# Optimization experiments

Measured on AMD Instinct MI355X. Metric: run time of the kernel, lower is better.

The kernel has to match this reference:

```python
import jax, jax.numpy as jnp
import numpy as np
from jax import lax

MARGIN = 0.3
BIGF = 1e9


def _pairwise_dist(x):
    # dist[i,j] = ||x_i - x_j||, clamped at 1e-12 before sqrt (as in torch code)
    sq = jnp.sum(x * x, axis=1)
    d = sq[:, None] + sq[None, :] - 2.0 * (x @ x.T)
    return jnp.sqrt(jnp.clip(d, 1e-12))


def _hard_mining(dist, targets):
    is_pos = targets[:, None] == targets[None, :]
    ap = jnp.where(is_pos, dist, jnp.asarray(-BIGF, dist.dtype))
    an = jnp.where(is_pos, jnp.asarray(BIGF, dist.dtype), dist)
    dist_ap = jnp.max(ap, axis=1)
    p_inds = jnp.argmax(ap, axis=1)
    dist_an = jnp.min(an, axis=1)
    n_inds = jnp.argmin(an, axis=1)
    return dist_ap, dist_an, p_inds, n_inds


def _batch_euclidean(x, y):
    # x: [N,m,d], y: [N,n,d] -> [N,m,n]
    xx = jnp.sum(x * x, axis=-1)[:, :, None]
    yy = jnp.sum(y * y, axis=-1)[:, None, :]
    d = xx + yy - 2.0 * jnp.einsum('nmd,nkd->nmk', x, y)
    return jnp.sqrt(jnp.clip(d, 1e-12))


def _shortest_dist(dmat):
    # DTW-style shortest path over [m,n] grid, batched over N: dp[i,j] = d[i,j] + min(dp[i-1,j], dp[i,j-1])
    N, m, n = dmat.shape
    big = jnp.asarray(BIGF, dmat.dtype)
    init_row = jnp.full((N, n), big, dmat.dtype).at[:, 0].set(0.0)  # virtual row -1: only (0,0) reachable

    def row_step(prev_row, drow):  # prev_row,drow: [N,n]
        def col_step(left, un):  # left: [N]
            up, d = un
            cur = d + jnp.minimum(up, left)
            return cur, cur
        _, cols = lax.scan(col_step, jnp.full((N,), big, dmat.dtype), (prev_row.T, drow.T))
        return cols.T, None

    last_row, _ = lax.scan(row_step, init_row, jnp.moveaxis(dmat, 1, 0))
    return last_row[:, -1]


def _batch_local_dist(x, y):
    d = _batch_euclidean(x, y)
    d = jnp.tanh(d * 0.5)  # == (exp(d)-1)/(exp(d)+1), numerically safe
    return _shortest_dist(d)


def _margin_ranking(dist_an, dist_ap, margin):
    # MarginRankingLoss with y=1: mean(relu(margin - (dist_an - dist_ap)))
    return jnp.mean(jnp.maximum(0.0, margin + dist_ap - dist_an))


def setup_inputs() -> dict:
    key = jax.random.key(0)
    k1, k2 = jax.random.split(key)
    N, D = 512, 2048
    LD, PARTS = 128, 8
    K = 4  # instances per identity (PK sampling)
    inputs = jax.random.normal(k1, (N, D), dtype=jnp.float32)
    local_features = jax.random.normal(k2, (N, LD, PARTS), dtype=jnp.float32)
    targets = jnp.arange(N, dtype=jnp.int64) // K
    return {"inputs": inputs, "targets": targets, "local_features": local_features}


def reference(inputs, targets, local_features):
    dist = _pairwise_dist(inputs)
    dist_ap, dist_an, p_inds, n_inds = _hard_mining(dist, targets)
    global_loss = _margin_ranking(dist_an, dist_ap, MARGIN)
    lf = jnp.transpose(local_features, (0, 2, 1))  # [N, parts, local_dim]
    local_ap = _batch_local_dist(lf, lf[p_inds])
    local_an = _batch_local_dist(lf, lf[n_inds])
    local_loss = _margin_ranking(local_an, local_ap, MARGIN)
    return (global_loss, local_loss)
```

## Files before the change

### kernel.cpp

```cpp
#include <hip/hip_runtime.h>
#include <math.h>

#define MARGIN 0.3f
#define BIGF 1e9f
#define NN 512
#define DD 2048
#define LDIM 128
#define PARTS 8

__global__ __launch_bounds__(256) void k_norms_init(
    const float* __restrict__ X, float* __restrict__ norms,
    float* gsum, float* lsum, unsigned* counter)
{
    int i = blockIdx.x;
    int t = threadIdx.x;
    const float4* xr = (const float4*)(X + (size_t)i * DD);
    float4 v1 = xr[t];
    float4 v2 = xr[t + 256];
    float acc = v1.x * v1.x + v1.y * v1.y + v1.z * v1.z + v1.w * v1.w
              + v2.x * v2.x + v2.y * v2.y + v2.z * v2.z + v2.w * v2.w;
    for (int off = 32; off > 0; off >>= 1)
        acc += __shfl_down(acc, off);
    __shared__ float part[4];
    int lane = t & 63, wid = t >> 6;
    if (lane == 0) part[wid] = acc;
    __syncthreads();
    if (t == 0) {
        norms[i] = part[0] + part[1] + part[2] + part[3];
        if (i == 0) { *gsum = 0.0f; *lsum = 0.0f; *counter = 0u; }
    }
}

__global__ __launch_bounds__(256) void k_gram(
    const float* __restrict__ X, float* __restrict__ Gp)
{
    __shared__ float As[16][64];
    __shared__ float Bs[16][64];
    int bid = blockIdx.x;
    int tj = bid & 7;
    int ti = (bid >> 3) & 7;
    int ks = bid >> 6;
    int tid = threadIdx.x;

    int lr = tid >> 2;
    int lc = (tid & 3) << 2;
    const float* Ap = X + (size_t)(ti * 64 + lr) * DD;
    const float* Bp = X + (size_t)(tj * 64 + lr) * DD;

    int ty = tid >> 4;
    int tx = tid & 15;

    float acc[4][4];
#pragma unroll
    for (int r = 0; r < 4; r++)
#pragma unroll
        for (int c = 0; c < 4; c++) acc[r][c] = 0.0f;

    int k0 = ks * 512;
    for (int kc = 0; kc < 32; kc++) {
        float4 av = *(const float4*)(Ap + k0 + lc);
        float4 bv = *(const float4*)(Bp + k0 + lc);
        __syncthreads();
        As[lc + 0][lr] = av.x; As[lc + 1][lr] = av.y;
        As[lc + 2][lr] = av.z; As[lc + 3][lr] = av.w;
        Bs[lc + 0][lr] = bv.x; Bs[lc + 1][lr] = bv.y;
        Bs[lc + 2][lr] = bv.z; Bs[lc + 3][lr] = bv.w;
        __syncthreads();
#pragma unroll
        for (int kk = 0; kk < 16; kk++) {
            float4 a4 = *(const float4*)&As[kk][ty << 2];
            float4 b4 = *(const float4*)&Bs[kk][tx << 2];
            float ar[4] = {a4.x, a4.y, a4.z, a4.w};
            float br[4] = {b4.x, b4.y, b4.z, b4.w};
#pragma unroll
            for (int r = 0; r < 4; r++)
#pragma unroll
                for (int c = 0; c < 4; c++)
                    acc[r][c] = fmaf(ar[r], br[c], acc[r][c]);
        }
        k0 += 16;
    }

    float* outp = Gp + (size_t)ks * NN * NN
                + (size_t)(ti * 64 + (ty << 2)) * NN + tj * 64 + (tx << 2);
#pragma unroll
    for (int r = 0; r < 4; r++) {
        float4 v = make_float4(acc[r][0], acc[r][1], acc[r][2], acc[r][3]);
        *(float4*)(outp + (size_t)r * NN) = v;
    }
}

__global__ __launch_bounds__(256) void k_mining(
    const float* __restrict__ Gp, const float* __restrict__ norms,
    const int* __restrict__ tg, int* __restrict__ p_inds,
    int* __restrict__ n_inds, float* gsum)
{
    int i = blockIdx.x;
    int t = threadIdx.x;
    float ni = norms[i];
    int tgt_i = tg[i];

    float apv = -BIGF; int api = 0x7fffffff;
    float anv =  BIGF; int ani = 0x7fffffff;

#pragma unroll
    for (int jj = 0; jj < 2; jj++) {
        int j = t + jj * 256;
        size_t base = (size_t)i * NN + j;
        float g = Gp[base] + Gp[base + (size_t)NN * NN]
                + Gp[base + 2ul * NN * NN] + Gp[base + 3ul * NN * NN];
        float dd = ni + norms[j] - 2.0f * g;
        float dist = sqrtf(fmaxf(dd, 1e-12f));
        bool pos = (tg[j] == tgt_i);
        float a = pos ? dist : -BIGF;
        if (a > apv || (a == apv && j < api)) { apv = a; api = j; }
        float b = pos ? BIGF : dist;
        if (b < anv || (b == anv && j < ani)) { anv = b; ani = j; }
    }
    for (int off = 32; off > 0; off >>= 1) {
        float av = __shfl_down(apv, off); int ai = __shfl_down(api, off);
        if (av > apv || (av == apv && ai < api)) { apv = av; api = ai; }
        float nv = __shfl_down(anv, off); int nid = __shfl_down(ani, off);
        if (nv < anv || (nv == anv && nid < ani)) { anv = nv; ani = nid; }
    }
    __shared__ float s_apv[4]; __shared__ int s_api[4];
    __shared__ float s_anv[4]; __shared__ int s_ani[4];
    int lane = t & 63, wid = t >> 6;
    if (lane == 0) { s_apv[wid] = apv; s_api[wid] = api;
                     s_anv[wid] = anv; s_ani[wid] = ani; }
    __syncthreads();
    if (t == 0) {
        apv = s_apv[0]; api = s_api[0]; anv = s_anv[0]; ani = s_ani[0];
        for (int wv = 1; wv < 4; wv++) {
            float av = s_apv[wv]; int ai = s_api[wv];
            if (av > apv || (av == apv && ai < api)) { apv = av; api = ai; }
            float nv = s_anv[wv]; int nid = s_ani[wv];
            if (nv < anv || (nv == anv && nid < ani)) { anv = nv; ani = nid; }
        }
        p_inds[i] = api;
        n_inds[i] = ani;
        atomicAdd(gsum, fmaxf(0.0f, MARGIN + apv - anv));
    }
}

__global__ __launch_bounds__(128) void k_local(
    const float* __restrict__ LF, const int* __restrict__ p_inds,
    const int* __restrict__ n_inds, const float* gsum, float* lsum,
    unsigned* counter, float* __restrict__ out)
{
    int i = blockIdx.x;
    int tid = threadIdx.x;
    int w = tid >> 6;
    int lane = tid & 63;

    __shared__ float A[LDIM * PARTS];
    __shared__ float B[2][LDIM * PARTS];
    __shared__ float dtm[2][64];
    __shared__ float res[2];

    const float4* A4 = (const float4*)(LF + (size_t)i * LDIM * PARTS);
    ((float4*)A)[tid]        = A4[tid];
    ((float4*)A)[tid + 128]  = A4[tid + 128];

    int ind = (w == 0) ? p_inds[i] : n_inds[i];
    const float4* B4 = (const float4*)(LF + (size_t)ind * LDIM * PARTS);
    float4* Bw = (float4*)B[w];
    Bw[lane]        = B4[lane];
    Bw[lane + 64]   = B4[lane + 64];
    Bw[lane + 128]  = B4[lane + 128];
    Bw[lane + 192]  = B4[lane + 192];
    __syncthreads();

    int p = lane >> 3, q = lane & 7;
    float acc = 0.0f;
    const float* Bl = B[w];
    for (int d = 0; d < LDIM; d++) {
        float diff = A[d * PARTS + p] - Bl[d * PARTS + q];
        acc = fmaf(diff, diff, acc);
    }
    float dist = sqrtf(fmaxf(acc, 1e-12f));
    dtm[w][p * 8 + q] = tanhf(0.5f * dist);
    __syncthreads();

    if (lane == 0) {
        const float* dm = dtm[w];
        float dp[8];
        dp[0] = dm[0];
        for (int j = 1; j < 8; j++) dp[j] = dp[j - 1] + dm[j];
        for (int r = 1; r < 8; r++) {
            dp[0] += dm[r * 8];
            for (int j = 1; j < 8; j++)
                dp[j] = dm[r * 8 + j] + fminf(dp[j], dp[j - 1]);
        }
        res[w] = dp[7];
    }
    __syncthreads();

    if (tid == 0) {
        float l = fmaxf(0.0f, MARGIN + res[0] - res[1]);
        atomicAdd(lsum, l);
        __threadfence();
        unsigned old = atomicAdd(counter, 1u);
        if (old == (NN - 1)) {
            float ls = atomicAdd(lsum, 0.0f);
            out[0] = (*(volatile const float*)gsum) * (1.0f / NN);
            out[1] = ls * (1.0f / NN);
        }
    }
}

extern "C" void kernel_launch(void* const* d_in, const int* in_sizes, int n_in,
                              void* d_out, int out_size, void* d_ws, size_t ws_size,
                              hipStream_t stream)
{
    const float* X  = (const float*)d_in[0];
    const int*   tg = (const int*)d_in[1];
    const float* LF = (const float*)d_in[2];
    float* out = (float*)d_out;

    char* ws = (char*)d_ws;
    float*    Gp      = (float*)ws;
    float*    norms   = (float*)(ws + 4194304);
    int*      p_inds  = (int*)  (ws + 4196352);
    int*      n_inds  = (int*)  (ws + 4198400);
    float*    gsum    = (float*)(ws + 4200448);
    float*    lsum    = (float*)(ws + 4200452);
    unsigned* counter = (unsigned*)(ws + 4200456);

    k_norms_init<<<NN, 256, 0, stream>>>(X, norms, gsum, lsum, counter);
    k_gram<<<256, 256, 0, stream>>>(X, Gp);
    k_mining<<<NN, 256, 0, stream>>>(Gp, norms, tg, p_inds, n_inds, gsum);
    k_local<<<NN, 128, 0, stream>>>(LF, p_inds, n_inds, gsum, lsum, counter, out);
}
```

Before: 115.2 us.

## Compute Gram matrix with split-bf16 MFMA and fuse mining with local loss

Input features are split into bf16 hi/lo parts in the prep kernel, and the Gram matrix is computed with 16x16x32 bf16 MFMA instructions using three products (hi*hi, hi*lo, lo*hi) to approximate fp32 accuracy. Tiles are loaded straight into LDS with global_load_lds. The mining and local-distance kernels are merged into one launch, so the p/n indices stay in shared memory and one kernel launch is removed. In exchange the prep kernel writes extra bf16 buffers, and the split-bf16 product is a small precision approximation of the fp32 Gram matrix.

```diff
diff --git a/kernel.cpp b/kernel.cpp
--- a/kernel.cpp
+++ b/kernel.cpp
@@ -8,9 +8,19 @@
 #define LDIM 128
 #define PARTS 8
 
-__global__ __launch_bounds__(256) void k_norms_init(
-    const float* __restrict__ X, float* __restrict__ norms,
-    float* gsum, float* lsum, unsigned* counter)
+typedef __attribute__((ext_vector_type(8))) __bf16 bf16x8;
+typedef __attribute__((ext_vector_type(4))) __bf16 bf16x4;
+typedef __attribute__((ext_vector_type(4))) float f32x4;
+
+__device__ __forceinline__ void load_lds16(const void* g, void* lds) {
+    __builtin_amdgcn_global_load_lds(
+        (const __attribute__((address_space(1))) unsigned int*)g,
+        (__attribute__((address_space(3))) unsigned int*)lds, 16, 0, 0);
+}
+
+__global__ __launch_bounds__(256) void k_prep(
+    const float* __restrict__ X, __bf16* __restrict__ Hhi, __bf16* __restrict__ Hlo,
+    float* __restrict__ norms, float* gsum, float* lsum, unsigned* counter)
 {
     int i = blockIdx.x;
     int t = threadIdx.x;
@@ -19,6 +29,24 @@
     float4 v2 = xr[t + 256];
     float acc = v1.x * v1.x + v1.y * v1.y + v1.z * v1.z + v1.w * v1.w
               + v2.x * v2.x + v2.y * v2.y + v2.z * v2.z + v2.w * v2.w;
+
+    float e1[4] = {v1.x, v1.y, v1.z, v1.w};
+    float e2[4] = {v2.x, v2.y, v2.z, v2.w};
+    bf16x4 h1, h2, l1, l2;
+#pragma unroll
+    for (int j = 0; j < 4; j++) {
+        __bf16 h = (__bf16)e1[j];
+        h1[j] = h;
+        l1[j] = (__bf16)(e1[j] - (float)h);
+        __bf16 g = (__bf16)e2[j];
+        h2[j] = g;
+        l2[j] = (__bf16)(e2[j] - (float)g);
+    }
+    bf16x4* hr = (bf16x4*)(Hhi + (size_t)i * DD);
+    bf16x4* lr = (bf16x4*)(Hlo + (size_t)i * DD);
+    hr[t] = h1; hr[t + 256] = h2;
+    lr[t] = l1; lr[t + 256] = l2;
+
     for (int off = 32; off > 0; off >>= 1)
         acc += __shfl_down(acc, off);
     __shared__ float part[4];
@@ -31,70 +59,98 @@
     }
 }
 
-__global__ __launch_bounds__(256) void k_gram(
-    const float* __restrict__ X, float* __restrict__ Gp)
-{
-    __shared__ float As[16][64];
-    __shared__ float Bs[16][64];
+__global__ __launch_bounds__(256) void k_gram_mfma(
+    const __bf16* __restrict__ Hhi, const __bf16* __restrict__ Hlo,
+    float* __restrict__ Gp)
+{
+    __shared__ __bf16 Ah[2048], Al[2048], Bh[2048], Bl[2048];
+
     int bid = blockIdx.x;
     int tj = bid & 7;
     int ti = (bid >> 3) & 7;
     int ks = bid >> 6;
-    int tid = threadIdx.x;
-
-    int lr = tid >> 2;
-    int lc = (tid & 3) << 2;
-    const float* Ap = X + (size_t)(ti * 64 + lr) * DD;
-    const float* Bp = X + (size_t)(tj * 64 + lr) * DD;
-
-    int ty = tid >> 4;
-    int tx = tid & 15;
-
-    float acc[4][4];
-#pragma unroll
-    for (int r = 0; r < 4; r++)
-#pragma unroll
-        for (int c = 0; c < 4; c++) acc[r][c] = 0.0f;
-
-    int k0 = ks * 512;
-    for (int kc = 0; kc < 32; kc++) {
-        float4 av = *(const float4*)(Ap + k0 + lc);
-        float4 bv = *(const float4*)(Bp + k0 + lc);
+    int t = threadIdx.x;
+    int w = t >> 6, lane = t & 63;
+    int wr = w >> 1, wc = w & 1;
+
+    int row16 = (w << 4) + (lane & 15);
+    int kchunk = (lane >> 4) << 3;
+    size_t kc0 = (size_t)(ks * 512 + kchunk);
+    const __bf16* pAh = Hhi + (size_t)(ti * 64 + row16) * DD + kc0;
+    const __bf16* pAl = Hlo + (size_t)(ti * 64 + row16) * DD + kc0;
+    const __bf16* pBh = Hhi + (size_t)(tj * 64 + row16) * DD + kc0;
+    const __bf16* pBl = Hlo + (size_t)(tj * 64 + row16) * DD + kc0;
+    __bf16* ldsAh = &Ah[w * 512];
+    __bf16* ldsAl = &Al[w * 512];
+    __bf16* ldsBh = &Bh[w * 512];
+    __bf16* ldsBl = &Bl[w * 512];
+
+    f32x4 acc00 = {0.f, 0.f, 0.f, 0.f};
+    f32x4 acc01 = {0.f, 0.f, 0.f, 0.f};
+    f32x4 acc10 = {0.f, 0.f, 0.f, 0.f};
+    f32x4 acc11 = {0.f, 0.f, 0.f, 0.f};
+
+    for (int it = 0; it < 16; ++it) {
+        load_lds16(pAh, ldsAh);
+        load_lds16(pBh, ldsBh);
+        load_lds16(pAl, ldsAl);
+        load_lds16(pBl, ldsBl);
+        pAh += 32; pAl += 32; pBh += 32; pBl += 32;
         __syncthreads();
-        As[lc + 0][lr] = av.x; As[lc + 1][lr] = av.y;
-        As[lc + 2][lr] = av.z; As[lc + 3][lr] = av.w;
-        Bs[lc + 0][lr] = bv.x; Bs[lc + 1][lr] = bv.y;
-        Bs[lc + 2][lr] = bv.z; Bs[lc + 3][lr] = bv.w;
+
+        const bf16x8* fAh = (const bf16x8*)&Ah[wr * 1024];
+        const bf16x8* fAl = (const bf16x8*)&Al[wr * 1024];
+        const bf16x8* fBh = (const bf16x8*)&Bh[wc * 1024];
+        const bf16x8* fBl = (const bf16x8*)&Bl[wc * 1024];
+        bf16x8 ah0 = fAh[lane], ah1 = fAh[lane + 64];
+        bf16x8 al0 = fAl[lane], al1 = fAl[lane + 64];
+        bf16x8 bh0 = fBh[lane], bh1 = fBh[lane + 64];
+        bf16x8 bl0 = fBl[lane], bl1 = fBl[lane + 64];
+
+        acc00 = __builtin_amdgcn_mfma_f32_16x16x32_bf16(ah0, bh0, acc00, 0, 0, 0);
+        acc00 = __builtin_amdgcn_mfma_f32_16x16x32_bf16(ah0, bl0, acc00, 0, 0, 0);
+        acc00 = __builtin_amdgcn_mfma_f32_16x16x32_bf16(al0, bh0, acc00, 0, 0, 0);
+
+        acc01 = __builtin_amdgcn_mfma_f32_16x16x32_bf16(ah0, bh1, acc01, 0, 0, 0);
+        acc01 = __builtin_amdgcn_mfma_f32_16x16x32_bf16(ah0, bl1, acc01, 0, 0, 0);
+        acc01 = __builtin_amdgcn_mfma_f32_16x16x32_bf16(al0, bh1, acc01, 0, 0, 0);
+
+        acc10 = __builtin_amdgcn_mfma_f32_16x16x32_bf16(ah1, bh0, acc10, 0, 0, 0);
+        acc10 = __builtin_amdgcn_mfma_f32_16x16x32_bf16(ah1, bl0, acc10, 0, 0, 0);
+        acc10 = __builtin_amdgcn_mfma_f32_16x16x32_bf16(al1, bh0, acc10, 0, 0, 0);
+
+        acc11 = __builtin_amdgcn_mfma_f32_16x16x32_bf16(ah1, bh1, acc11, 0, 0, 0);
+        acc11 = __builtin_amdgcn_mfma_f32_16x16x32_bf16(ah1, bl1, acc11, 0, 0, 0);
+        acc11 = __builtin_amdgcn_mfma_f32_16x16x32_bf16(al1, bh1, acc11, 0, 0, 0);
         __syncthreads();
-#pragma unroll
-        for (int kk = 0; kk < 16; kk++) {
-            float4 a4 = *(const float4*)&As[kk][ty << 2];
-            float4 b4 = *(const float4*)&Bs[kk][tx << 2];
-            float ar[4] = {a4.x, a4.y, a4.z, a4.w};
-            float br[4] = {b4.x, b4.y, b4.z, b4.w};
+    }
+
+    int rbase = ti * 64 + wr * 32 + ((lane >> 4) << 2);
+    int cbase = tj * 64 + wc * 32 + (lane & 15);
+    float* gb = Gp + (size_t)ks * NN * NN;
+    f32x4 accs[2][2] = {{acc00, acc01}, {acc10, acc11}};
+#pragma unroll
+    for (int g = 0; g < 2; g++)
+#pragma unroll
+        for (int h = 0; h < 2; h++)
 #pragma unroll
             for (int r = 0; r < 4; r++)
-#pragma unroll
-                for (int c = 0; c < 4; c++)
-                    acc[r][c] = fmaf(ar[r], br[c], acc[r][c]);
-        }
-        k0 += 16;
-    }
-
-    float* outp = Gp + (size_t)ks * NN * NN
-                + (size_t)(ti * 64 + (ty << 2)) * NN + tj * 64 + (tx << 2);
-#pragma unroll
-    for (int r = 0; r < 4; r++) {
-        float4 v = make_float4(acc[r][0], acc[r][1], acc[r][2], acc[r][3]);
-        *(float4*)(outp + (size_t)r * NN) = v;
-    }
-}
-
-__global__ __launch_bounds__(256) void k_mining(
+                gb[(size_t)(rbase + g * 16 + r) * NN + cbase + h * 16] = accs[g][h][r];
+}
+
+__global__ __launch_bounds__(256) void k_mine_local(
     const float* __restrict__ Gp, const float* __restrict__ norms,
-    const int* __restrict__ tg, int* __restrict__ p_inds,
-    int* __restrict__ n_inds, float* gsum)
-{
+    const int* __restrict__ tg, const float* __restrict__ LF,
+    float* gsum, float* lsum, unsigned* counter, float* __restrict__ out)
+{
+    __shared__ float s_apv[4]; __shared__ int s_api[4];
+    __shared__ float s_anv[4]; __shared__ int s_ani[4];
+    __shared__ int sh_pn[2];
+    __shared__ float A[LDIM * PARTS];
+    __shared__ float B[2][LDIM * PARTS];
+    __shared__ float dtm[2][64];
+    __shared__ float res[2];
+
     int i = blockIdx.x;
     int t = threadIdx.x;
     float ni = norms[i];
@@ -123,8 +179,6 @@
         float nv = __shfl_down(anv, off); int nid = __shfl_down(ani, off);
         if (nv < anv || (nv == anv && nid < ani)) { anv = nv; ani = nid; }
     }
-    __shared__ float s_apv[4]; __shared__ int s_api[4];
-    __shared__ float s_anv[4]; __shared__ int s_ani[4];
     int lane = t & 63, wid = t >> 6;
     if (lane == 0) { s_apv[wid] = apv; s_api[wid] = api;
                      s_anv[wid] = anv; s_ani[wid] = ani; }
@@ -137,52 +191,39 @@
             float nv = s_anv[wv]; int nid = s_ani[wv];
             if (nv < anv || (nv == anv && nid < ani)) { anv = nv; ani = nid; }
         }
-        p_inds[i] = api;
-        n_inds[i] = ani;
+        sh_pn[0] = api;
+        sh_pn[1] = ani;
         atomicAdd(gsum, fmaxf(0.0f, MARGIN + apv - anv));
     }
-}
-
-__global__ __launch_bounds__(128) void k_local(
-    const float* __restrict__ LF, const int* __restrict__ p_inds,
-    const int* __restrict__ n_inds, const float* gsum, float* lsum,
-    unsigned* counter, float* __restrict__ out)
-{
-    int i = blockIdx.x;
-    int tid = threadIdx.x;
-    int w = tid >> 6;
-    int lane = tid & 63;
-
-    __shared__ float A[LDIM * PARTS];
-    __shared__ float B[2][LDIM * PARTS];
-    __shared__ float dtm[2][64];
-    __shared__ float res[2];
-
-    const float4* A4 = (const float4*)(LF + (size_t)i * LDIM * PARTS);
-    ((float4*)A)[tid]        = A4[tid];
-    ((float4*)A)[tid + 128]  = A4[tid + 128];
-
-    int ind = (w == 0) ? p_inds[i] : n_inds[i];
-    const float4* B4 = (const float4*)(LF + (size_t)ind * LDIM * PARTS);
-    float4* Bw = (float4*)B[w];
-    Bw[lane]        = B4[lane];
-    Bw[lane + 64]   = B4[lane + 64];
-    Bw[lane + 128]  = B4[lane + 128];
-    Bw[lane + 192]  = B4[lane + 192];
-    __syncthreads();
-
-    int p = lane >> 3, q = lane & 7;
-    float acc = 0.0f;
-    const float* Bl = B[w];
-    for (int d = 0; d < LDIM; d++) {
-        float diff = A[d * PARTS + p] - Bl[d * PARTS + q];
-        acc = fmaf(diff, diff, acc);
-    }
-    float dist = sqrtf(fmaxf(acc, 1e-12f));
-    dtm[w][p * 8 + q] = tanhf(0.5f * dist);
-    __syncthreads();
-
-    if (lane == 0) {
+    __syncthreads();
+
+    int w = t >> 6;
+    ((float4*)A)[t] = ((const float4*)(LF + (size_t)i * LDIM * PARTS))[t];
+    if (w < 2) {
+        int ind = sh_pn[w];
+        const float4* B4 = (const float4*)(LF + (size_t)ind * LDIM * PARTS);
+        float4* Bw = (float4*)B[w];
+        Bw[lane]       = B4[lane];
+        Bw[lane + 64]  = B4[lane + 64];
+        Bw[lane + 128] = B4[lane + 128];
+        Bw[lane + 192] = B4[lane + 192];
+    }
+    __syncthreads();
+
+    if (w < 2) {
+        int p = lane >> 3, q = lane & 7;
+        float acc = 0.0f;
+        const float* Bw = B[w];
+        for (int d = 0; d < LDIM; d++) {
+            float diff = A[d * PARTS + p] - Bw[d * PARTS + q];
+            acc = fmaf(diff, diff, acc);
+        }
+        float dist = sqrtf(fmaxf(acc, 1e-12f));
+        dtm[w][p * 8 + q] = tanhf(0.5f * dist);
+    }
+    __syncthreads();
+
+    if ((t == 0) || (t == 64)) {
         const float* dm = dtm[w];
         float dp[8];
         dp[0] = dm[0];
@@ -196,14 +237,16 @@
     }
     __syncthreads();
 
-    if (tid == 0) {
+    if (t == 0) {
         float l = fmaxf(0.0f, MARGIN + res[0] - res[1]);
         atomicAdd(lsum, l);
         __threadfence();
         unsigned old = atomicAdd(counter, 1u);
         if (old == (NN - 1)) {
+            __threadfence();
             float ls = atomicAdd(lsum, 0.0f);
-            out[0] = (*(volatile const float*)gsum) * (1.0f / NN);
+            float gs = atomicAdd(gsum, 0.0f);
+            out[0] = gs * (1.0f / NN);
             out[1] = ls * (1.0f / NN);
         }
     }
@@ -220,15 +263,14 @@
 
     char* ws = (char*)d_ws;
     float*    Gp      = (float*)ws;
-    float*    norms   = (float*)(ws + 4194304);
-    int*      p_inds  = (int*)  (ws + 4196352);
-    int*      n_inds  = (int*)  (ws + 4198400);
-    float*    gsum    = (float*)(ws + 4200448);
-    float*    lsum    = (float*)(ws + 4200452);
-    unsigned* counter = (unsigned*)(ws + 4200456);
-
-    k_norms_init<<<NN, 256, 0, stream>>>(X, norms, gsum, lsum, counter);
-    k_gram<<<256, 256, 0, stream>>>(X, Gp);
-    k_mining<<<NN, 256, 0, stream>>>(Gp, norms, tg, p_inds, n_inds, gsum);
-    k_local<<<NN, 128, 0, stream>>>(LF, p_inds, n_inds, gsum, lsum, counter, out);
-}
+    __bf16*   Hhi     = (__bf16*)(ws + (4u << 20));
+    __bf16*   Hlo     = (__bf16*)(ws + (6u << 20));
+    float*    norms   = (float*)(ws + (8u << 20));
+    float*    gsum    = (float*)(ws + (8u << 20) + 4096);
+    float*    lsum    = (float*)(ws + (8u << 20) + 4100);
+    unsigned* counter = (unsigned*)(ws + (8u << 20) + 4104);
+
+    k_prep<<<NN, 256, 0, stream>>>(X, Hhi, Hlo, norms, gsum, lsum, counter);
+    k_gram_mfma<<<256, 256, 0, stream>>>(Hhi, Hlo, Gp);
+    k_mine_local<<<NN, 256, 0, stream>>>(Gp, norms, tg, LF, gsum, lsum, counter, out);
+}
```

Result: faster. 100.3 us (-13.0%).
